# Kernel tuning notes

Hardware: AMD Instinct MI355X
Metric: run time of the kernel (lower is better)

Reference implementation:

```python
import jax, jax.numpy as jnp
import numpy as np

B, C, H, W = 8, 128, 128, 128
WS, NH = 4, 8
HD = C // NH
SCALE = HD ** -0.5
HG, WG = H // WS, W // WS
G, N = HG * WG, WS * WS


def conv2d(x, w, b, padding=0, groups=1):
    out = jax.lax.conv_general_dilated(
        x, w, (1, 1), [(padding, padding)] * 2,
        dimension_numbers=('NCHW', 'OIHW', 'NCHW'),
        feature_group_count=groups)
    return out + b[None, :, None, None]


def dsc(x, dw_w, dw_b, pw_w, pw_b):
    # depthwise 3x3 (groups=C) then pointwise 1x1
    h = conv2d(x, dw_w, dw_b, padding=1, groups=x.shape[1])
    return conv2d(h, pw_w, pw_b)


def _window(t):
    # (B,C,H,W) -> (B,G,NH,N,HD) exactly as torch reshape/permute
    t = t.reshape(B, NH, HD, HG, WS, WG, WS)
    return t.transpose(0, 3, 5, 1, 4, 6, 2).reshape(B, G, NH, N, HD)


def setup_inputs() -> dict:
    key = jax.random.key(0)
    ks = jax.random.split(key, 32)
    s = 0.02
    Cr = max(C // 8, 1)
    d = {
        'x': jax.random.normal(ks[0], (B, C, H, W), jnp.float32),
        'y': jax.random.normal(ks[1], (B, C, H, W), jnp.float32),
        'ca_w1': jax.random.normal(ks[2], (Cr, 2 * C, 1, 1)) * s,
        'ca_b1': jnp.zeros((Cr,)),
        'ca_w2': jax.random.normal(ks[3], (2 * C, Cr, 1, 1)) * s,
        'ca_b2': jnp.zeros((2 * C,)),
        'final_w': jax.random.normal(ks[4], (C, 3 * C, 1, 1)) * s,
        'final_b': jnp.zeros((C,)),
        'bn_g': jnp.ones((C,)),
        'bn_b': jnp.zeros((C,)),
        'bn_m': jnp.zeros((C,)),
        'bn_v': jnp.ones((C,)),
    }
    for i, name in enumerate(['q', 'k', 'v', 'proj']):
        d[name + '_dw_w'] = jax.random.normal(ks[5 + 4 * i], (C, 1, 3, 3)) * s
        d[name + '_dw_b'] = jnp.zeros((C,))
        d[name + '_pw_w'] = jax.random.normal(ks[6 + 4 * i], (C, C, 1, 1)) * s
        d[name + '_pw_b'] = jnp.zeros((C,))
    return d


def reference(x, y, ca_w1, ca_b1, ca_w2, ca_b2,
              q_dw_w, q_dw_b, q_pw_w, q_pw_b,
              k_dw_w, k_dw_b, k_pw_w, k_pw_b,
              v_dw_w, v_dw_b, v_pw_w, v_pw_b,
              proj_dw_w, proj_dw_b, proj_pw_w, proj_pw_b,
              final_w, final_b, bn_g, bn_b, bn_m, bn_v):
    element_wise = x * y
    concat = jnp.concatenate([x, y], axis=1)  # (B,2C,H,W)
    # channel attention (squeeze-excite)
    pooled = concat.mean(axis=(2, 3), keepdims=True)
    h = jax.nn.relu(conv2d(pooled, ca_w1, ca_b1))
    ca = jax.nn.sigmoid(conv2d(h, ca_w2, ca_b2))
    attended = concat * ca
    x_att, y_att = attended[:, :C], attended[:, C:]
    # windowed cross-attention: q from y_att, k/v from x_att
    q = _window(dsc(y_att, q_dw_w, q_dw_b, q_pw_w, q_pw_b))
    k = _window(dsc(x_att, k_dw_w, k_dw_b, k_pw_w, k_pw_b))
    v = _window(dsc(x_att, v_dw_w, v_dw_b, v_pw_w, v_pw_b))
    attn = jnp.einsum('bgnqd,bgnkd->bgnqk', q, k) * SCALE
    attn = jax.nn.softmax(attn, axis=-1)
    out = jnp.einsum('bgnqk,bgnkd->bgnqd', attn, v)  # (B,G,NH,N,HD)
    out = out.transpose(0, 1, 3, 2, 4).reshape(B, HG, WG, WS, WS, C)
    out = out.transpose(0, 1, 3, 2, 4, 5).reshape(B, H, W, C).transpose(0, 3, 1, 2)
    cross = dsc(out, proj_dw_w, proj_dw_b, proj_pw_w, proj_pw_b)
    fused = jnp.concatenate([element_wise, y_att, cross], axis=1)
    z = conv2d(fused, final_w, final_b)
    # BatchNorm in eval mode with running stats
    inv = jax.lax.rsqrt(bn_v + 1e-5)
    z = (z - bn_m[None, :, None, None]) * (inv * bn_g)[None, :, None, None] + bn_b[None, :, None, None]
    return jax.nn.relu(z)
```

## Files before the change

kernel.cpp:

```cpp
#include <hip/hip_runtime.h>

typedef __attribute__((ext_vector_type(8))) short short8;
typedef __attribute__((ext_vector_type(4))) float f32x4;
typedef __attribute__((ext_vector_type(2))) unsigned u32x2;
typedef __attribute__((ext_vector_type(4))) unsigned u32x4;

static constexpr int C_ = 128, H_ = 128, W_ = 128;
static constexpr int HW_ = H_ * W_;
static constexpr int CHW_ = C_ * HW_;

__device__ __forceinline__ unsigned short f2b(float f) {
  union { float f; unsigned u; } cv; cv.f = f;
  unsigned r = cv.u + 0x7FFFu + ((cv.u >> 16) & 1u);
  return (unsigned short)(r >> 16);
}
__device__ __forceinline__ float b2f(unsigned short h) {
  union { unsigned u; float f; } cv; cv.u = ((unsigned)h) << 16;
  return cv.f;
}
__device__ __forceinline__ float uasf(unsigned u) {
  union { unsigned u; float f; } cv; cv.u = u; return cv.f;
}
__device__ __forceinline__ int swzo(int pos, int byteInRow) {
  return pos * 256 + (byteInRow ^ ((pos & 7) << 4));
}

__global__ __launch_bounds__(256) void k_pool(const float* __restrict__ x,
                                              const float* __restrict__ y,
                                              float* __restrict__ sums) {
  int blk = blockIdx.x;
  int b = blk >> 8, c = blk & 255;
  const float* src = (c < C_) ? (x + (size_t)b * CHW_ + (size_t)c * HW_)
                              : (y + (size_t)b * CHW_ + (size_t)(c - C_) * HW_);
  const float4* s4 = (const float4*)src;
  float acc = 0.f;
  for (int i = threadIdx.x; i < HW_ / 4; i += 256) {
    float4 v = s4[i];
    acc += v.x + v.y + v.z + v.w;
  }
  for (int off = 32; off; off >>= 1) acc += __shfl_down(acc, off, 64);
  __shared__ float red[4];
  int lane = threadIdx.x & 63, wv = threadIdx.x >> 6;
  if (lane == 0) red[wv] = acc;
  __syncthreads();
  if (threadIdx.x == 0) sums[blk] = red[0] + red[1] + red[2] + red[3];
}

__global__ __launch_bounds__(256) void k_ca(const float* __restrict__ sums,
                                            const float* __restrict__ w1,
                                            const float* __restrict__ b1,
                                            const float* __restrict__ w2,
                                            const float* __restrict__ b2,
                                            float* __restrict__ ca) {
  int b = blockIdx.x;
  __shared__ float pooled[256];
  __shared__ float hb[16];
  int t = threadIdx.x;
  pooled[t] = sums[b * 256 + t] * (1.f / 16384.f);
  __syncthreads();
  if (t < 16) {
    float s = b1[t];
    for (int j = 0; j < 256; ++j) s += w1[t * 256 + j] * pooled[j];
    hb[t] = fmaxf(s, 0.f);
  }
  __syncthreads();
  float s = b2[t];
  for (int r = 0; r < 16; ++r) s += w2[t * 16 + r] * hb[r];
  ca[b * 256 + t] = 1.f / (1.f + __expf(-s));
}

__global__ __launch_bounds__(128) void k_prep(
    const float* __restrict__ qpw, const float* __restrict__ kpw,
    const float* __restrict__ vpw,
    const float* __restrict__ fw, const float* __restrict__ fb,
    const float* __restrict__ ppw, const float* __restrict__ ppb,
    const float* __restrict__ cab,
    unsigned short* __restrict__ Wb, unsigned short* __restrict__ W2b,
    float* __restrict__ bc) {
  int blk = blockIdx.x, c = threadIdx.x;
  if (blk < 768) {
    int mat = blk >> 7, o = blk & 127;
    float v = 0.f;
    if (mat == 0) v = qpw[o * 128 + c];
    else if (mat == 1) v = kpw[o * 128 + c];
    else if (mat == 2) v = vpw[o * 128 + c];
    else if (mat == 3) {
      float a = 0.f;
      for (int m = 0; m < 128; ++m) a += fw[o * 384 + 256 + m] * ppw[m * 128 + c];
      v = a;
      if (c == 0) {
        float bb = fb[o];
        for (int m = 0; m < 128; ++m) bb += fw[o * 384 + 256 + m] * ppb[m];
        bc[o] = bb;
      }
    } else if (mat == 4) v = fw[o * 384 + c];
    else v = 0.f;
    Wb[((size_t)mat << 14) + o * 128 + c] = f2b(v);
  } else {
    int bb = (blk - 768) >> 7, o = blk & 127;
    W2b[((size_t)bb << 14) + o * 128 + c] =
        f2b(fw[o * 384 + 128 + c] * cab[bb * 256 + 128 + c]);
  }
}

__global__ __launch_bounds__(512, 4) void k_qkv_attn(
    const float* __restrict__ x, const float* __restrict__ y,
    const float* __restrict__ cab,
    const float* __restrict__ qdw, const float* __restrict__ qdb,
    const float* __restrict__ kdw, const float* __restrict__ kdb,
    const float* __restrict__ vdw, const float* __restrict__ vdb,
    const unsigned short* __restrict__ Wqkv,
    const float* __restrict__ qpb, const float* __restrict__ kpb,
    const float* __restrict__ vpb,
    unsigned short* __restrict__ outb) {
  __shared__ __align__(16) char lds[53248];
  constexpr int QS = 0, OS = 0;
  constexpr int AV = 16384, VT = 16384;
  constexpr int AK = 32768, KS = 32768;
  constexpr int HA = 16384;
  constexpr int SCR = 49152;

  const int t = threadIdx.x;
  const int l = t & 63;
  const int w = t >> 6;
  const int lm = l & 15, g = l >> 4;
  const int bs = ((blockIdx.x & 7) << 8) | (blockIdx.x >> 3);
  const int b = bs >> 8, tr = bs & 255;
  const int y0 = (tr >> 3) << 2, x0 = (tr & 7) << 4;
  const int ct = t & 127, rowt = t >> 7;
  const int mtile = w & 3, nbase = (w >> 2) * 64;
  unsigned short* hal = (unsigned short*)(lds + HA);

  auto halo_direct = [&](const float* src) {
    #pragma unroll
    for (int tk = 0; tk < 2; ++tk) {
      int task = t + tk * 512;
      if (task < 768) {
        int c = task & 127, hr = task >> 7;
        int gy = y0 - 1 + hr;
        bool rowok = (unsigned)gy < 128u;
        const float* rsrc = src + (size_t)c * HW_ + (size_t)gy * W_;
        f32x4 v[6];
        #pragma unroll
        for (int ck = 0; ck < 6; ++ck) {
          int gx0 = x0 - 4 + 4 * ck;
          bool ok2 = rowok && ((unsigned)gx0 < 125u);
          v[ck] = ok2 ? *(const f32x4*)(rsrc + gx0) : f32x4{0.f, 0.f, 0.f, 0.f};
        }
        int base = (hr * 128 + c) * 18;
        const float* f = (const float*)v;
        #pragma unroll
        for (int e = 0; e < 9; ++e) {
          unsigned u = (unsigned)f2b(f[2 * e + 3]) |
                       ((unsigned)f2b(f[2 * e + 4]) << 16);
          *(unsigned*)(hal + base + 2 * e) = u;
        }
      }
    }
  };

  auto dw_q = [&](const float* wdw, const float* bdw, const float* cas) {
    const float* wp = wdw + ct * 9;
    float wr[9];
    #pragma unroll
    for (int k2 = 0; k2 < 9; ++k2) wr[k2] = wp[k2];
    float cam = cas[ct], bb = bdw[ct];
    float o[16];
    #pragma unroll
    for (int px = 0; px < 16; ++px) o[px] = 0.f;
    #pragma unroll
    for (int rr = 0; rr < 3; ++rr) {
      int base = ((rowt + rr) * 128 + ct) * 18;
      unsigned rp[9];
      #pragma unroll
      for (int e = 0; e < 9; ++e) rp[e] = *(const unsigned*)(hal + base + 2 * e);
      float rv[18];
      #pragma unroll
      for (int e = 0; e < 9; ++e) {
        rv[2 * e] = uasf(rp[e] << 16);
        rv[2 * e + 1] = uasf(rp[e] & 0xffff0000u);
      }
      #pragma unroll
      for (int px = 0; px < 16; ++px)
        o[px] += rv[px] * wr[3 * rr] + rv[px + 1] * wr[3 * rr + 1] +
                 rv[px + 2] * wr[3 * rr + 2];
    }
    #pragma unroll
    for (int px = 0; px < 16; ++px)
      *(unsigned short*)(lds + QS + swzo(rowt * 16 + px, 2 * ct)) =
          f2b(o[px] * cam + bb);
  };

  auto dw_from_regs = [&](const unsigned* hx, const float* wdw,
                          const float* bdw, float cam, int dstOff) {
    const float* wp = wdw + ct * 9;
    float wr[9];
    #pragma unroll
    for (int k2 = 0; k2 < 9; ++k2) wr[k2] = wp[k2];
    float bb = bdw[ct];
    float o[16];
    #pragma unroll
    for (int px = 0; px < 16; ++px) o[px] = 0.f;
    #pragma unroll
    for (int rr = 0; rr < 3; ++rr) {
      float rv[18];
      #pragma unroll
      for (int e = 0; e < 9; ++e) {
        unsigned pk = hx[rr * 9 + e];
        rv[2 * e] = uasf(pk << 16);
        rv[2 * e + 1] = uasf(pk & 0xffff0000u);
      }
      #pragma unroll
      for (int px = 0; px < 16; ++px)
        o[px] += rv[px] * wr[3 * rr] + rv[px + 1] * wr[3 * rr + 1] +
                 rv[px + 2] * wr[3 * rr + 2];
    }
    #pragma unroll
    for (int px = 0; px < 16; ++px)
      *(unsigned short*)(lds + dstOff + swzo(rowt * 16 + px, 2 * ct)) =
          f2b(o[px] * cam + bb);
  };

  auto afrag_load = [&](int aOff, short8* a) {
    #pragma unroll
    for (int ks = 0; ks < 4; ++ks)
      a[ks] = *(const short8*)(lds + aOff +
                 swzo(mtile * 16 + lm, ks * 64 + g * 16));
  };
  auto gemm_from = [&](const short8* a, const unsigned short* Wm,
                       const float* bias, int dstOff) {
    f32x4 acc[4];
    #pragma unroll
    for (int nt = 0; nt < 4; ++nt) acc[nt] = f32x4{0.f, 0.f, 0.f, 0.f};
    #pragma unroll
    for (int ks = 0; ks < 4; ++ks) {
      short8 wf[4];
      #pragma unroll
      for (int nt = 0; nt < 4; ++nt)
        wf[nt] = *(const short8*)(Wm + (nbase + nt * 16 + lm) * 128 +
                                  ks * 32 + g * 8);
      #pragma unroll
      for (int nt = 0; nt < 4; ++nt)
        acc[nt] = __builtin_amdgcn_mfma_f32_16x16x32_bf16(a[ks], wf[nt], acc[nt], 0, 0, 0);
    }
    #pragma unroll
    for (int nt = 0; nt < 4; ++nt) {
      int ch = nbase + nt * 16 + lm;
      float bv = bias[ch];
      #pragma unroll
      for (int r2 = 0; r2 < 4; ++r2) {
        int pos = mtile * 16 + g * 4 + r2;
        *(unsigned short*)(lds + dstOff + swzo(pos, 2 * ch)) =
            f2b(acc[nt][r2] + bv);
      }
    }
  };
  auto gemm_v_from = [&](const short8* a, const unsigned short* Wm,
                         const float* bias) {
    f32x4 acc[4];
    #pragma unroll
    for (int nt = 0; nt < 4; ++nt) acc[nt] = f32x4{0.f, 0.f, 0.f, 0.f};
    #pragma unroll
    for (int ks = 0; ks < 4; ++ks) {
      short8 wf[4];
      #pragma unroll
      for (int nt = 0; nt < 4; ++nt)
        wf[nt] = *(const short8*)(Wm + (nbase + nt * 16 + lm) * 128 +
                                  ks * 32 + g * 8);
      #pragma unroll
      for (int nt = 0; nt < 4; ++nt)
        acc[nt] = __builtin_amdgcn_mfma_f32_16x16x32_bf16(a[ks], wf[nt], acc[nt], 0, 0, 0);
    }
    #pragma unroll
    for (int nt = 0; nt < 4; ++nt) {
      int ch = nbase + nt * 16 + lm;
      float bv = bias[ch];
      int col = (g * 16 + mtile * 4) ^ ((ch & 7) << 3);
      unsigned lo = (unsigned)f2b(acc[nt][0] + bv) |
                    ((unsigned)f2b(acc[nt][1] + bv) << 16);
      unsigned hi = (unsigned)f2b(acc[nt][2] + bv) |
                    ((unsigned)f2b(acc[nt][3] + bv) << 16);
      *(u32x2*)(lds + VT + ch * 128 + 2 * col) = u32x2{lo, hi};
    }
  };

  const float* cax = cab + b * 256;
  const float* cay = cax + 128;
  const float* xb = x + (size_t)b * CHW_;
  const float* yb = y + (size_t)b * CHW_;

  halo_direct(yb);
  __syncthreads();
  dw_q(qdw, qdb, cay);
  __syncthreads();
  short8 aq[4];
  afrag_load(QS, aq);
  halo_direct(xb);
  __syncthreads();
  gemm_from(aq, Wqkv, qpb, QS);
  __builtin_amdgcn_sched_barrier(0);
  unsigned hx[27];
  #pragma unroll
  for (int rr = 0; rr < 3; ++rr) {
    int base = ((rowt + rr) * 128 + ct) * 18;
    #pragma unroll
    for (int e = 0; e < 9; ++e)
      hx[rr * 9 + e] = *(const unsigned*)(hal + base + 2 * e);
  }
  __syncthreads();
  {
    float cam = cax[ct];
    dw_from_regs(hx, kdw, kdb, cam, AK);
    dw_from_regs(hx, vdw, vdb, cam, AV);
  }
  __syncthreads();
  short8 ak[4], av4[4];
  afrag_load(AK, ak);
  afrag_load(AV, av4);
  __syncthreads();
  gemm_from(ak, Wqkv + 16384, kpb, KS);
  gemm_v_from(av4, Wqkv + 32768, vpb);
  __syncthreads();

  u32x2 oac[4];
  {
    const int h = w;
    const int chb = h * 32;
    char* scr = lds + SCR + w * 512;
    const short8 zz = {};
    #pragma unroll
    for (int wi = 0; wi < 4; ++wi) {
      int rowp = (lm >> 2) * 16 + wi * 4 + (lm & 3);
      short8 avf = zz, bvf = zz;
      if (g < 2) {
        avf = *(const short8*)(lds + KS + swzo(rowp, chb + g * 16));
        bvf = *(const short8*)(lds + QS + swzo(rowp, chb + g * 16));
      }
      f32x4 st = __builtin_amdgcn_mfma_f32_16x16x32_bf16(
          avf, bvf, f32x4{0.f, 0.f, 0.f, 0.f}, 0, 0, 0);
      float s0 = st[0] * 0.25f, s1 = st[1] * 0.25f,
            s2 = st[2] * 0.25f, s3 = st[3] * 0.25f;
      float mx = fmaxf(fmaxf(s0, s1), fmaxf(s2, s3));
      mx = fmaxf(mx, __shfl_xor(mx, 16, 64));
      mx = fmaxf(mx, __shfl_xor(mx, 32, 64));
      float e0 = __expf(s0 - mx), e1 = __expf(s1 - mx),
            e2 = __expf(s2 - mx), e3 = __expf(s3 - mx);
      float sm = e0 + e1 + e2 + e3;
      sm += __shfl_xor(sm, 16, 64);
      sm += __shfl_xor(sm, 32, 64);
      float rl = 1.f / sm;
      unsigned p0 = (unsigned)f2b(e0 * rl) | ((unsigned)f2b(e1 * rl) << 16);
      unsigned p1 = (unsigned)f2b(e2 * rl) | ((unsigned)f2b(e3 * rl) << 16);
      *(u32x2*)(scr + lm * 32 + g * 8) = u32x2{p0, p1};
      short8 pb2 = zz, va = zz;
      if (g < 2) {
        pb2 = *(const short8*)(scr + lm * 32 + g * 16);
        int ch = h * 16 + lm;
        va = *(const short8*)(lds + VT + ch * 128 +
                              2 * ((wi * 16 + g * 8) ^ ((ch & 7) << 3)));
      }
      f32x4 ot = __builtin_amdgcn_mfma_f32_16x16x32_bf16(
          va, pb2, f32x4{0.f, 0.f, 0.f, 0.f}, 0, 0, 0);
      unsigned o0 = (unsigned)f2b(ot[0]) | ((unsigned)f2b(ot[1]) << 16);
      unsigned o1 = (unsigned)f2b(ot[2]) | ((unsigned)f2b(ot[3]) << 16);
      oac[wi] = u32x2{o0, o1};
    }
  }
  __syncthreads();
  {
    const int chb = w * 32;
    #pragma unroll
    for (int wi = 0; wi < 4; ++wi) {
      int rowp = (lm >> 2) * 16 + wi * 4 + (lm & 3);
      *(u32x2*)(lds + OS + swzo(rowp, chb + g * 8)) = oac[wi];
    }
  }
  __syncthreads();
  {
    unsigned short* dst = outb + (size_t)b * CHW_ + (size_t)ct * HW_ +
                          (y0 + rowt) * W_ + x0;
    unsigned v[8];
    #pragma unroll
    for (int j = 0; j < 8; ++j) {
      unsigned lo = *(const unsigned short*)(lds + OS + swzo(rowt * 16 + 2 * j, 2 * ct));
      unsigned hi = *(const unsigned short*)(lds + OS + swzo(rowt * 16 + 2 * j + 1, 2 * ct));
      v[j] = lo | (hi << 16);
    }
    *(u32x4*)(dst) = u32x4{v[0], v[1], v[2], v[3]};
    *(u32x4*)(dst + 8) = u32x4{v[4], v[5], v[6], v[7]};
  }
}

__global__ __launch_bounds__(512, 4) void k_final(
    const float* __restrict__ x, const float* __restrict__ y,
    const unsigned short* __restrict__ outb,
    const float* __restrict__ pdw, const float* __restrict__ pdb,
    const unsigned short* __restrict__ W3,
    const unsigned short* __restrict__ W2b,
    const float* __restrict__ bc,
    const float* __restrict__ bng, const float* __restrict__ bnb,
    const float* __restrict__ bnm, const float* __restrict__ bnv,
    float* __restrict__ outp) {
  __shared__ __align__(16) char lds[50176];
  constexpr int A1 = 0, HA = 16384;

  const int t = threadIdx.x, l = t & 63, w = t >> 6;
  const int lm = l & 15, g = l >> 4;
  const int bs = ((blockIdx.x & 7) << 8) | (blockIdx.x >> 3);
  const int b = bs >> 8, tr = bs & 255;
  const int y0 = (tr >> 3) << 2, x0 = (tr & 7) << 4;
  const int ct = t & 127, rowt = t >> 7;
  unsigned short* hal = (unsigned short*)(lds + HA);
  const int mtile = w & 3, nbase = (w >> 2) * 64;

  f32x4 acc[4];
  #pragma unroll
  for (int nt = 0; nt < 4; ++nt) acc[nt] = f32x4{0.f, 0.f, 0.f, 0.f};

  auto gemm_acc = [&](const unsigned short* Wm) {
    #pragma unroll
    for (int ks = 0; ks < 4; ++ks) {
      short8 wf[4];
      #pragma unroll
      for (int nt = 0; nt < 4; ++nt)
        wf[nt] = *(const short8*)(Wm + (nbase + nt * 16 + lm) * 128 +
                                  ks * 32 + g * 8);
      short8 a = *(const short8*)(lds + A1 +
                   swzo(mtile * 16 + lm, ks * 64 + g * 16));
      #pragma unroll
      for (int nt = 0; nt < 4; ++nt)
        acc[nt] = __builtin_amdgcn_mfma_f32_16x16x32_bf16(a, wf[nt], acc[nt], 0, 0, 0);
    }
  };

  const size_t gbase = (size_t)b * CHW_ + (size_t)ct * HW_ +
                       (size_t)(y0 + rowt) * W_ + x0;

  #pragma unroll
  for (int e = 0; e < 4; ++e) {
    f32x4 xv = *(const f32x4*)(x + gbase + 4 * e);
    f32x4 yv = *(const f32x4*)(y + gbase + 4 * e);
    #pragma unroll
    for (int j = 0; j < 4; ++j)
      *(unsigned short*)(lds + A1 + swzo(rowt * 16 + 4 * e + j, 2 * ct)) =
          f2b(xv[j] * yv[j]);
  }
  #pragma unroll
  for (int tk = 0; tk < 2; ++tk) {
    int task = t + tk * 512;
    if (task < 768) {
      int c = task & 127, hr = task >> 7;
      int gy = y0 - 1 + hr;
      bool rowok = (unsigned)gy < 128u;
      const unsigned short* hsrc =
          outb + (size_t)b * CHW_ + (size_t)c * HW_ + (size_t)gy * W_;
      int base = (hr * 128 + c) * 22;
      #pragma unroll
      for (int e = 0; e < 10; ++e) {
        int gx0 = x0 - 2 + 2 * e;
        bool okp = rowok && ((unsigned)gx0 < 127u);
        unsigned u = okp ? *(const unsigned*)(hsrc + gx0) : 0u;
        *(unsigned*)(hal + base + 2 * e) = u;
      }
    }
  }
  __syncthreads();
  gemm_acc(W3 + 16384);
  __syncthreads();
  #pragma unroll
  for (int e = 0; e < 4; ++e) {
    f32x4 yv = *(const f32x4*)(y + gbase + 4 * e);
    #pragma unroll
    for (int j = 0; j < 4; ++j)
      *(unsigned short*)(lds + A1 + swzo(rowt * 16 + 4 * e + j, 2 * ct)) =
          f2b(yv[j]);
  }
  __syncthreads();
  gemm_acc(W2b + ((size_t)b << 14));
  __syncthreads();
  {
    const float* wp = pdw + ct * 9;
    float wr[9];
    #pragma unroll
    for (int k2 = 0; k2 < 9; ++k2) wr[k2] = wp[k2];
    float bb = pdb[ct];
    #pragma unroll
    for (int hf = 0; hf < 2; ++hf) {
      float o[8];
      #pragma unroll
      for (int px = 0; px < 8; ++px) o[px] = 0.f;
      #pragma unroll
      for (int rr = 0; rr < 3; ++rr) {
        int base = ((rowt + rr) * 128 + ct) * 22 + 8 * hf;
        unsigned rp[6];
        #pragma unroll
        for (int e = 0; e < 6; ++e)
          rp[e] = *(const unsigned*)(hal + base + 2 * e);
        float rv[12];
        #pragma unroll
        for (int e = 0; e < 6; ++e) {
          rv[2 * e] = uasf(rp[e] << 16);
          rv[2 * e + 1] = uasf(rp[e] & 0xffff0000u);
        }
        #pragma unroll
        for (int px = 0; px < 8; ++px)
          o[px] += rv[px + 1] * wr[3 * rr] + rv[px + 2] * wr[3 * rr + 1] +
                   rv[px + 3] * wr[3 * rr + 2];
      }
      #pragma unroll
      for (int px = 0; px < 8; ++px)
        *(unsigned short*)(lds + A1 + swzo(rowt * 16 + hf * 8 + px, 2 * ct)) =
            f2b(o[px] + bb);
    }
  }
  __syncthreads();
  gemm_acc(W3);
  float* fst = (float*)(lds + HA);
  #pragma unroll
  for (int nt = 0; nt < 4; ++nt) {
    int ch = nbase + nt * 16 + lm;
    float zb = bc[ch];
    float inv = rsqrtf(bnv[ch] + 1e-5f);
    float gsc = inv * bng[ch];
    float mm = bnm[ch], ab = bnb[ch];
    #pragma unroll
    for (int r2 = 0; r2 < 4; ++r2) {
      int pos = mtile * 16 + g * 4 + r2;
      float z = acc[nt][r2] + zb;
      z = (z - mm) * gsc + ab;
      fst[pos * 130 + ch] = fmaxf(z, 0.f);
    }
  }
  __syncthreads();
  #pragma unroll
  for (int e4 = 0; e4 < 4; ++e4) {
    f32x4 ov;
    #pragma unroll
    for (int j = 0; j < 4; ++j) ov[j] = fst[(rowt * 16 + e4 * 4 + j) * 130 + ct];
    *(f32x4*)(outp + gbase + 4 * e4) = ov;
  }
}

extern "C" void kernel_launch(void* const* d_in, const int* in_sizes, int n_in,
                              void* d_out, int out_size, void* d_ws, size_t ws_size,
                              hipStream_t stream) {
  const float* x       = (const float*)d_in[0];
  const float* y       = (const float*)d_in[1];
  const float* ca_w1   = (const float*)d_in[2];
  const float* ca_b1   = (const float*)d_in[3];
  const float* ca_w2   = (const float*)d_in[4];
  const float* ca_b2   = (const float*)d_in[5];
  const float* final_w = (const float*)d_in[6];
  const float* final_b = (const float*)d_in[7];
  const float* bn_g    = (const float*)d_in[8];
  const float* bn_b    = (const float*)d_in[9];
  const float* bn_m    = (const float*)d_in[10];
  const float* bn_v    = (const float*)d_in[11];
  const float* q_dw_w  = (const float*)d_in[12];
  const float* q_dw_b  = (const float*)d_in[13];
  const float* q_pw_w  = (const float*)d_in[14];
  const float* q_pw_b  = (const float*)d_in[15];
  const float* k_dw_w  = (const float*)d_in[16];
  const float* k_dw_b  = (const float*)d_in[17];
  const float* k_pw_w  = (const float*)d_in[18];
  const float* k_pw_b  = (const float*)d_in[19];
  const float* v_dw_w  = (const float*)d_in[20];
  const float* v_dw_b  = (const float*)d_in[21];
  const float* v_pw_w  = (const float*)d_in[22];
  const float* v_pw_b  = (const float*)d_in[23];
  const float* p_dw_w  = (const float*)d_in[24];
  const float* p_dw_b  = (const float*)d_in[25];
  const float* p_pw_w  = (const float*)d_in[26];
  const float* p_pw_b  = (const float*)d_in[27];

  char* ws = (char*)d_ws;
  float* sums = (float*)(ws + 0);
  float* cab  = (float*)(ws + 8192);
  unsigned short* Wqkv = (unsigned short*)(ws + 16384);
  unsigned short* W3   = Wqkv + 3 * 16384;
  float* bc   = (float*)(ws + 212992);
  unsigned short* W2b  = (unsigned short*)(ws + 213504);
  unsigned short* outb = (unsigned short*)(ws + (1 << 20));

  k_pool<<<2048, 256, 0, stream>>>(x, y, sums);
  k_ca<<<8, 256, 0, stream>>>(sums, ca_w1, ca_b1, ca_w2, ca_b2, cab);
  k_prep<<<1792, 128, 0, stream>>>(q_pw_w, k_pw_w, v_pw_w, final_w, final_b,
                                   p_pw_w, p_pw_b, cab, Wqkv, W2b, bc);
  k_qkv_attn<<<2048, 512, 0, stream>>>(x, y, cab,
      q_dw_w, q_dw_b, k_dw_w, k_dw_b, v_dw_w, v_dw_b,
      Wqkv, q_pw_b, k_pw_b, v_pw_b, outb);
  k_final<<<2048, 512, 0, stream>>>(x, y, outb,
      p_dw_w, p_dw_b, W3, W2b, bc,
      bn_g, bn_b, bn_m, bn_v, (float*)d_out);
}
```

Before: 376.8 us.

## Halve spatial tiles to 32 pixels with 256-thread blocks in both main kernels

Both fused kernels now process 32-pixel tiles (4x8 for attention, 2x16 for final) with 256 threads and half the LDS, launched as 4096 blocks instead of 2048. The depthwise stage is restructured so each thread computes two output rows from four halo rows, and the V-transpose layout is simplified per window. The block index now puts batch in the low bits. The aim is higher occupancy and better latency hiding. The cost is more halo overhead per pixel (a larger fraction of redundant border loads) and more blocks to schedule.

Result: slower. 427.8 us (+13.5%).

```diff
diff --git a/kernel.cpp b/kernel.cpp
--- a/kernel.cpp
+++ b/kernel.cpp
@@ -13,10 +13,6 @@
   union { float f; unsigned u; } cv; cv.f = f;
   unsigned r = cv.u + 0x7FFFu + ((cv.u >> 16) & 1u);
   return (unsigned short)(r >> 16);
-}
-__device__ __forceinline__ float b2f(unsigned short h) {
-  union { unsigned u; float f; } cv; cv.u = ((unsigned)h) << 16;
-  return cv.f;
 }
 __device__ __forceinline__ float uasf(unsigned u) {
   union { unsigned u; float f; } cv; cv.u = u; return cv.f;
@@ -103,7 +99,7 @@
   }
 }
 
-__global__ __launch_bounds__(512, 4) void k_qkv_attn(
+__global__ __launch_bounds__(256, 6) void k_qkv_attn(
     const float* __restrict__ x, const float* __restrict__ y,
     const float* __restrict__ cab,
     const float* __restrict__ qdw, const float* __restrict__ qdb,
@@ -113,112 +109,133 @@
     const float* __restrict__ qpb, const float* __restrict__ kpb,
     const float* __restrict__ vpb,
     unsigned short* __restrict__ outb) {
-  __shared__ __align__(16) char lds[53248];
+  __shared__ __align__(16) char lds[26624];
   constexpr int QS = 0, OS = 0;
-  constexpr int AV = 16384, VT = 16384;
-  constexpr int AK = 32768, KS = 32768;
-  constexpr int HA = 16384;
-  constexpr int SCR = 49152;
+  constexpr int AV = 8192, VT = 8192;
+  constexpr int AK = 16384, KS = 16384;
+  constexpr int HA = 8192;
+  constexpr int SCR = 24576;
 
   const int t = threadIdx.x;
-  const int l = t & 63;
-  const int w = t >> 6;
+  const int l = t & 63, w = t >> 6;
   const int lm = l & 15, g = l >> 4;
-  const int bs = ((blockIdx.x & 7) << 8) | (blockIdx.x >> 3);
-  const int b = bs >> 8, tr = bs & 255;
-  const int y0 = (tr >> 3) << 2, x0 = (tr & 7) << 4;
-  const int ct = t & 127, rowt = t >> 7;
-  const int mtile = w & 3, nbase = (w >> 2) * 64;
+  const int blk = blockIdx.x;
+  const int b = blk & 7, r = blk >> 3;
+  const int ty = r >> 4, tx = r & 15;
+  const int y0 = ty << 2, x0 = tx << 3;
+  const int ct = t & 127, rt = t >> 7;
+  const int mtile = w & 1, nbase = (w >> 1) * 64;
   unsigned short* hal = (unsigned short*)(lds + HA);
 
   auto halo_direct = [&](const float* src) {
     #pragma unroll
-    for (int tk = 0; tk < 2; ++tk) {
-      int task = t + tk * 512;
-      if (task < 768) {
-        int c = task & 127, hr = task >> 7;
-        int gy = y0 - 1 + hr;
-        bool rowok = (unsigned)gy < 128u;
-        const float* rsrc = src + (size_t)c * HW_ + (size_t)gy * W_;
-        f32x4 v[6];
-        #pragma unroll
-        for (int ck = 0; ck < 6; ++ck) {
-          int gx0 = x0 - 4 + 4 * ck;
-          bool ok2 = rowok && ((unsigned)gx0 < 125u);
-          v[ck] = ok2 ? *(const f32x4*)(rsrc + gx0) : f32x4{0.f, 0.f, 0.f, 0.f};
-        }
-        int base = (hr * 128 + c) * 18;
-        const float* f = (const float*)v;
-        #pragma unroll
-        for (int e = 0; e < 9; ++e) {
-          unsigned u = (unsigned)f2b(f[2 * e + 3]) |
-                       ((unsigned)f2b(f[2 * e + 4]) << 16);
-          *(unsigned*)(hal + base + 2 * e) = u;
-        }
+    for (int tk = 0; tk < 3; ++tk) {
+      int task = t + tk * 256;
+      int c = task & 127, hr = task >> 7;
+      int gy = y0 - 1 + hr;
+      bool rowok = (unsigned)gy < 128u;
+      const float* rsrc = src + (size_t)c * HW_ + (size_t)gy * W_;
+      f32x4 v[4];
+      #pragma unroll
+      for (int ck = 0; ck < 4; ++ck) {
+        int gx0 = x0 - 4 + 4 * ck;
+        bool ok2 = rowok && ((unsigned)gx0 < 125u);
+        v[ck] = ok2 ? *(const f32x4*)(rsrc + gx0) : f32x4{0.f, 0.f, 0.f, 0.f};
+      }
+      int base = task * 10;
+      const float* f = (const float*)v;
+      #pragma unroll
+      for (int e = 0; e < 5; ++e) {
+        unsigned u = (unsigned)f2b(f[2 * e + 3]) |
+                     ((unsigned)f2b(f[2 * e + 4]) << 16);
+        *(unsigned*)(hal + base + 2 * e) = u;
       }
     }
   };
 
-  auto dw_q = [&](const float* wdw, const float* bdw, const float* cas) {
+  auto dw_q2 = [&](const float* wdw, const float* bdw, const float* cas,
+                   int dstOff) {
     const float* wp = wdw + ct * 9;
     float wr[9];
     #pragma unroll
     for (int k2 = 0; k2 < 9; ++k2) wr[k2] = wp[k2];
+    float o0[8], o1[8];
+    #pragma unroll
+    for (int px = 0; px < 8; ++px) { o0[px] = 0.f; o1[px] = 0.f; }
+    #pragma unroll
+    for (int rr = 0; rr < 4; ++rr) {
+      int base = ((2 * rt + rr) * 128 + ct) * 10;
+      float rv[10];
+      #pragma unroll
+      for (int e = 0; e < 5; ++e) {
+        unsigned pk = *(const unsigned*)(hal + base + 2 * e);
+        rv[2 * e] = uasf(pk << 16);
+        rv[2 * e + 1] = uasf(pk & 0xffff0000u);
+      }
+      if (rr < 3) {
+        #pragma unroll
+        for (int px = 0; px < 8; ++px)
+          o0[px] += rv[px] * wr[3 * rr] + rv[px + 1] * wr[3 * rr + 1] +
+                    rv[px + 2] * wr[3 * rr + 2];
+      }
+      if (rr > 0) {
+        int rq = rr - 1;
+        #pragma unroll
+        for (int px = 0; px < 8; ++px)
+          o1[px] += rv[px] * wr[3 * rq] + rv[px + 1] * wr[3 * rq + 1] +
+                    rv[px + 2] * wr[3 * rq + 2];
+      }
+    }
     float cam = cas[ct], bb = bdw[ct];
-    float o[16];
-    #pragma unroll
-    for (int px = 0; px < 16; ++px) o[px] = 0.f;
-    #pragma unroll
-    for (int rr = 0; rr < 3; ++rr) {
-      int base = ((rowt + rr) * 128 + ct) * 18;
-      unsigned rp[9];
-      #pragma unroll
-      for (int e = 0; e < 9; ++e) rp[e] = *(const unsigned*)(hal + base + 2 * e);
-      float rv[18];
-      #pragma unroll
-      for (int e = 0; e < 9; ++e) {
-        rv[2 * e] = uasf(rp[e] << 16);
-        rv[2 * e + 1] = uasf(rp[e] & 0xffff0000u);
-      }
-      #pragma unroll
-      for (int px = 0; px < 16; ++px)
-        o[px] += rv[px] * wr[3 * rr] + rv[px + 1] * wr[3 * rr + 1] +
-                 rv[px + 2] * wr[3 * rr + 2];
-    }
-    #pragma unroll
-    for (int px = 0; px < 16; ++px)
-      *(unsigned short*)(lds + QS + swzo(rowt * 16 + px, 2 * ct)) =
-          f2b(o[px] * cam + bb);
+    #pragma unroll
+    for (int px = 0; px < 8; ++px) {
+      *(unsigned short*)(lds + dstOff + swzo(2 * rt * 8 + px, 2 * ct)) =
+          f2b(o0[px] * cam + bb);
+      *(unsigned short*)(lds + dstOff + swzo((2 * rt + 1) * 8 + px, 2 * ct)) =
+          f2b(o1[px] * cam + bb);
+    }
   };
 
-  auto dw_from_regs = [&](const unsigned* hx, const float* wdw,
-                          const float* bdw, float cam, int dstOff) {
+  auto dw_from_hx = [&](const unsigned* hx, const float* wdw,
+                        const float* bdw, float cam, int dstOff) {
     const float* wp = wdw + ct * 9;
     float wr[9];
     #pragma unroll
     for (int k2 = 0; k2 < 9; ++k2) wr[k2] = wp[k2];
-    float bb = bdw[ct];
-    float o[16];
-    #pragma unroll
-    for (int px = 0; px < 16; ++px) o[px] = 0.f;
-    #pragma unroll
-    for (int rr = 0; rr < 3; ++rr) {
-      float rv[18];
-      #pragma unroll
-      for (int e = 0; e < 9; ++e) {
-        unsigned pk = hx[rr * 9 + e];
+    float o0[8], o1[8];
+    #pragma unroll
+    for (int px = 0; px < 8; ++px) { o0[px] = 0.f; o1[px] = 0.f; }
+    #pragma unroll
+    for (int rr = 0; rr < 4; ++rr) {
+      float rv[10];
+      #pragma unroll
+      for (int e = 0; e < 5; ++e) {
+        unsigned pk = hx[rr * 5 + e];
         rv[2 * e] = uasf(pk << 16);
         rv[2 * e + 1] = uasf(pk & 0xffff0000u);
       }
-      #pragma unroll
-      for (int px = 0; px < 16; ++px)
-        o[px] += rv[px] * wr[3 * rr] + rv[px + 1] * wr[3 * rr + 1] +
-                 rv[px + 2] * wr[3 * rr + 2];
-    }
-    #pragma unroll
-    for (int px = 0; px < 16; ++px)
-      *(unsigned short*)(lds + dstOff + swzo(rowt * 16 + px, 2 * ct)) =
-          f2b(o[px] * cam + bb);
+      if (rr < 3) {
+        #pragma unroll
+        for (int px = 0; px < 8; ++px)
+          o0[px] += rv[px] * wr[3 * rr] + rv[px + 1] * wr[3 * rr + 1] +
+                    rv[px + 2] * wr[3 * rr + 2];
+      }
+      if (rr > 0) {
+        int rq = rr - 1;
+        #pragma unroll
+        for (int px = 0; px < 8; ++px)
+          o1[px] += rv[px] * wr[3 * rq] + rv[px + 1] * wr[3 * rq + 1] +
+                    rv[px + 2] * wr[3 * rq + 2];
+      }
+    }
+    float bb = bdw[ct];
+    #pragma unroll
+    for (int px = 0; px < 8; ++px) {
+      *(unsigned short*)(lds + dstOff + swzo(2 * rt * 8 + px, 2 * ct)) =
+          f2b(o0[px] * cam + bb);
+      *(unsigned short*)(lds + dstOff + swzo((2 * rt + 1) * 8 + px, 2 * ct)) =
+          f2b(o1[px] * cam + bb);
+    }
   };
 
   auto afrag_load = [&](int aOff, short8* a) {
@@ -248,10 +265,10 @@
       int ch = nbase + nt * 16 + lm;
       float bv = bias[ch];
       #pragma unroll
-      for (int r2 = 0; r2 < 4; ++r2) {
-        int pos = mtile * 16 + g * 4 + r2;
+      for (int rr = 0; rr < 4; ++rr) {
+        int pos = mtile * 16 + g * 4 + rr;
         *(unsigned short*)(lds + dstOff + swzo(pos, 2 * ch)) =
-            f2b(acc[nt][r2] + bv);
+            f2b(acc[nt][rr] + bv);
       }
     }
   };
@@ -271,16 +288,17 @@
       for (int nt = 0; nt < 4; ++nt)
         acc[nt] = __builtin_amdgcn_mfma_f32_16x16x32_bf16(a[ks], wf[nt], acc[nt], 0, 0, 0);
     }
+    int win = g & 1;
+    int kpb = mtile * 8 + (g >> 1) * 4;
     #pragma unroll
     for (int nt = 0; nt < 4; ++nt) {
       int ch = nbase + nt * 16 + lm;
       float bv = bias[ch];
-      int col = (g * 16 + mtile * 4) ^ ((ch & 7) << 3);
       unsigned lo = (unsigned)f2b(acc[nt][0] + bv) |
                     ((unsigned)f2b(acc[nt][1] + bv) << 16);
       unsigned hi = (unsigned)f2b(acc[nt][2] + bv) |
                     ((unsigned)f2b(acc[nt][3] + bv) << 16);
-      *(u32x2*)(lds + VT + ch * 128 + 2 * col) = u32x2{lo, hi};
+      *(u32x2*)(lds + VT + win * 4096 + ch * 32 + 2 * kpb) = u32x2{lo, hi};
     }
   };
 
@@ -291,27 +309,26 @@
 
   halo_direct(yb);
   __syncthreads();
-  dw_q(qdw, qdb, cay);
+  dw_q2(qdw, qdb, cay, QS);
   __syncthreads();
   short8 aq[4];
   afrag_load(QS, aq);
   halo_direct(xb);
   __syncthreads();
   gemm_from(aq, Wqkv, qpb, QS);
-  __builtin_amdgcn_sched_barrier(0);
-  unsigned hx[27];
+  unsigned hx[20];
   #pragma unroll
-  for (int rr = 0; rr < 3; ++rr) {
-    int base = ((rowt + rr) * 128 + ct) * 18;
-    #pragma unroll
-    for (int e = 0; e < 9; ++e)
-      hx[rr * 9 + e] = *(const unsigned*)(hal + base + 2 * e);
+  for (int rr = 0; rr < 4; ++rr) {
+    int base = ((2 * rt + rr) * 128 + ct) * 10;
+    #pragma unroll
+    for (int e = 0; e < 5; ++e)
+      hx[rr * 5 + e] = *(const unsigned*)(hal + base + 2 * e);
   }
   __syncthreads();
   {
     float cam = cax[ct];
-    dw_from_regs(hx, kdw, kdb, cam, AK);
-    dw_from_regs(hx, vdw, vdb, cam, AV);
+    dw_from_hx(hx, kdw, kdb, cam, AK);
+    dw_from_hx(hx, vdw, vdb, cam, AV);
   }
   __syncthreads();
   short8 ak[4], av4[4];
@@ -324,13 +341,13 @@
 
   u32x2 oac[4];
   {
-    const int h = w;
-    const int chb = h * 32;
     char* scr = lds + SCR + w * 512;
     const short8 zz = {};
     #pragma unroll
     for (int wi = 0; wi < 4; ++wi) {
-      int rowp = (lm >> 2) * 16 + wi * 4 + (lm & 3);
+      int win = wi & 1, h = w * 2 + (wi >> 1);
+      int chb = h * 32;
+      int rowp = (lm >> 2) * 8 + win * 4 + (lm & 3);
       short8 avf = zz, bvf = zz;
       if (g < 2) {
         avf = *(const short8*)(lds + KS + swzo(rowp, chb + g * 16));
@@ -356,8 +373,7 @@
       if (g < 2) {
         pb2 = *(const short8*)(scr + lm * 32 + g * 16);
         int ch = h * 16 + lm;
-        va = *(const short8*)(lds + VT + ch * 128 +
-                              2 * ((wi * 16 + g * 8) ^ ((ch & 7) << 3)));
+        va = *(const short8*)(lds + VT + win * 4096 + ch * 32 + g * 16);
       }
       f32x4 ot = __builtin_amdgcn_mfma_f32_16x16x32_bf16(
           va, pb2, f32x4{0.f, 0.f, 0.f, 0.f}, 0, 0, 0);
@@ -368,30 +384,32 @@
   }
   __syncthreads();
   {
-    const int chb = w * 32;
     #pragma unroll
     for (int wi = 0; wi < 4; ++wi) {
-      int rowp = (lm >> 2) * 16 + wi * 4 + (lm & 3);
-      *(u32x2*)(lds + OS + swzo(rowp, chb + g * 8)) = oac[wi];
+      int win = wi & 1, h = w * 2 + (wi >> 1);
+      int rowp = (lm >> 2) * 8 + win * 4 + (lm & 3);
+      *(u32x2*)(lds + OS + swzo(rowp, h * 32 + g * 8)) = oac[wi];
     }
   }
   __syncthreads();
   {
-    unsigned short* dst = outb + (size_t)b * CHW_ + (size_t)ct * HW_ +
-                          (y0 + rowt) * W_ + x0;
-    unsigned v[8];
-    #pragma unroll
-    for (int j = 0; j < 8; ++j) {
-      unsigned lo = *(const unsigned short*)(lds + OS + swzo(rowt * 16 + 2 * j, 2 * ct));
-      unsigned hi = *(const unsigned short*)(lds + OS + swzo(rowt * 16 + 2 * j + 1, 2 * ct));
-      v[j] = lo | (hi << 16);
-    }
-    *(u32x4*)(dst) = u32x4{v[0], v[1], v[2], v[3]};
-    *(u32x4*)(dst + 8) = u32x4{v[4], v[5], v[6], v[7]};
-  }
-}
-
-__global__ __launch_bounds__(512, 4) void k_final(
+    unsigned short* dst = outb + (size_t)b * CHW_ + (size_t)ct * HW_;
+    #pragma unroll
+    for (int i = 0; i < 2; ++i) {
+      int py = 2 * rt + i;
+      unsigned v[4];
+      #pragma unroll
+      for (int j = 0; j < 4; ++j) {
+        unsigned lo = *(const unsigned short*)(lds + OS + swzo(py * 8 + 2 * j, 2 * ct));
+        unsigned hi = *(const unsigned short*)(lds + OS + swzo(py * 8 + 2 * j + 1, 2 * ct));
+        v[j] = lo | (hi << 16);
+      }
+      *(u32x4*)(dst + (size_t)(y0 + py) * W_ + x0) = u32x4{v[0], v[1], v[2], v[3]};
+    }
+  }
+}
+
+__global__ __launch_bounds__(256, 5) void k_final(
     const float* __restrict__ x, const float* __restrict__ y,
     const unsigned short* __restrict__ outb,
     const float* __restrict__ pdw, const float* __restrict__ pdb,
@@ -401,17 +419,19 @@
     const float* __restrict__ bng, const float* __restrict__ bnb,
     const float* __restrict__ bnm, const float* __restrict__ bnv,
     float* __restrict__ outp) {
-  __shared__ __align__(16) char lds[50176];
-  constexpr int A1 = 0, HA = 16384;
-
-  const int t = threadIdx.x, l = t & 63, w = t >> 6;
+  __shared__ __align__(16) char lds[28672];
+  constexpr int A1 = 0, HA = 8192;
+
+  const int t = threadIdx.x;
+  const int l = t & 63, w = t >> 6;
   const int lm = l & 15, g = l >> 4;
-  const int bs = ((blockIdx.x & 7) << 8) | (blockIdx.x >> 3);
-  const int b = bs >> 8, tr = bs & 255;
-  const int y0 = (tr >> 3) << 2, x0 = (tr & 7) << 4;
-  const int ct = t & 127, rowt = t >> 7;
+  const int blk = blockIdx.x;
+  const int b = blk & 7, r = blk >> 3;
+  const int ty = r >> 3, tx = r & 7;
+  const int y0 = ty << 1, x0 = tx << 4;
+  const int ct = t & 127, rt = t >> 7;
   unsigned short* hal = (unsigned short*)(lds + HA);
-  const int mtile = w & 3, nbase = (w >> 2) * 64;
+  const int mtile = w & 1, nbase = (w >> 1) * 64;
 
   f32x4 acc[4];
   #pragma unroll
@@ -434,7 +454,7 @@
   };
 
   const size_t gbase = (size_t)b * CHW_ + (size_t)ct * HW_ +
-                       (size_t)(y0 + rowt) * W_ + x0;
+                       (size_t)(y0 + rt) * W_ + x0;
 
   #pragma unroll
   for (int e = 0; e < 4; ++e) {
@@ -442,26 +462,24 @@
     f32x4 yv = *(const f32x4*)(y + gbase + 4 * e);
     #pragma unroll
     for (int j = 0; j < 4; ++j)
-      *(unsigned short*)(lds + A1 + swzo(rowt * 16 + 4 * e + j, 2 * ct)) =
+      *(unsigned short*)(lds + A1 + swzo(rt * 16 + 4 * e + j, 2 * ct)) =
           f2b(xv[j] * yv[j]);
   }
   #pragma unroll
   for (int tk = 0; tk < 2; ++tk) {
-    int task = t + tk * 512;
-    if (task < 768) {
-      int c = task & 127, hr = task >> 7;
-      int gy = y0 - 1 + hr;
-      bool rowok = (unsigned)gy < 128u;
-      const unsigned short* hsrc =
-          outb + (size_t)b * CHW_ + (size_t)c * HW_ + (size_t)gy * W_;
-      int base = (hr * 128 + c) * 22;
-      #pragma unroll
-      for (int e = 0; e < 10; ++e) {
-        int gx0 = x0 - 2 + 2 * e;
-        bool okp = rowok && ((unsigned)gx0 < 127u);
-        unsigned u = okp ? *(const unsigned*)(hsrc + gx0) : 0u;
-        *(unsigned*)(hal + base + 2 * e) = u;
-      }
+    int task = t + tk * 256;
+    int c = task & 127, hr = task >> 7;
+    int gy = y0 - 1 + hr;
+    bool rowok = (unsigned)gy < 128u;
+    const unsigned short* hsrc =
+        outb + (size_t)b * CHW_ + (size_t)c * HW_ + (size_t)gy * W_;
+    int base = task * 20;
+    #pragma unroll
+    for (int e = 0; e < 10; ++e) {
+      int gx0 = x0 - 2 + 2 * e;
+      bool okp = rowok && ((unsigned)gx0 < 127u);
+      unsigned u = okp ? *(const unsigned*)(hsrc + gx0) : 0u;
+      *(unsigned*)(hal + base + 2 * e) = u;
     }
   }
   __syncthreads();
@@ -472,7 +490,7 @@
     f32x4 yv = *(const f32x4*)(y + gbase + 4 * e);
     #pragma unroll
     for (int j = 0; j < 4; ++j)
-      *(unsigned short*)(lds + A1 + swzo(rowt * 16 + 4 * e + j, 2 * ct)) =
+      *(unsigned short*)(lds + A1 + swzo(rt * 16 + 4 * e + j, 2 * ct)) =
           f2b(yv[j]);
   }
   __syncthreads();
@@ -484,34 +502,28 @@
     #pragma unroll
     for (int k2 = 0; k2 < 9; ++k2) wr[k2] = wp[k2];
     float bb = pdb[ct];
-    #pragma unroll
-    for (int hf = 0; hf < 2; ++hf) {
-      float o[8];
-      #pragma unroll
-      for (int px = 0; px < 8; ++px) o[px] = 0.f;
-      #pragma unroll
-      for (int rr = 0; rr < 3; ++rr) {
-        int base = ((rowt + rr) * 128 + ct) * 22 + 8 * hf;
-        unsigned rp[6];
-        #pragma unroll
-        for (int e = 0; e < 6; ++e)
-          rp[e] = *(const unsigned*)(hal + base + 2 * e);
-        float rv[12];
-        #pragma unroll
-        for (int e = 0; e < 6; ++e) {
-          rv[2 * e] = uasf(rp[e] << 16);
-          rv[2 * e + 1] = uasf(rp[e] & 0xffff0000u);
-        }
-        #pragma unroll
-        for (int px = 0; px < 8; ++px)
-          o[px] += rv[px + 1] * wr[3 * rr] + rv[px + 2] * wr[3 * rr + 1] +
-                   rv[px + 3] * wr[3 * rr + 2];
-      }
-      #pragma unroll
-      for (int px = 0; px < 8; ++px)
-        *(unsigned short*)(lds + A1 + swzo(rowt * 16 + hf * 8 + px, 2 * ct)) =
-            f2b(o[px] + bb);
-    }
+    float o[16];
+    #pragma unroll
+    for (int px = 0; px < 16; ++px) o[px] = 0.f;
+    #pragma unroll
+    for (int rr = 0; rr < 3; ++rr) {
+      int base = ((rt + rr) * 128 + ct) * 20;
+      float rv[20];
+      #pragma unroll
+      for (int e = 0; e < 10; ++e) {
+        unsigned pk = *(const unsigned*)(hal + base + 2 * e);
+        rv[2 * e] = uasf(pk << 16);
+        rv[2 * e + 1] = uasf(pk & 0xffff0000u);
+      }
+      #pragma unroll
+      for (int px = 0; px < 16; ++px)
+        o[px] += rv[px + 1] * wr[3 * rr] + rv[px + 2] * wr[3 * rr + 1] +
+                 rv[px + 3] * wr[3 * rr + 2];
+    }
+    #pragma unroll
+    for (int px = 0; px < 16; ++px)
+      *(unsigned short*)(lds + A1 + swzo(rt * 16 + px, 2 * ct)) =
+          f2b(o[px] + bb);
   }
   __syncthreads();
   gemm_acc(W3);
@@ -524,9 +536,9 @@
     float gsc = inv * bng[ch];
     float mm = bnm[ch], ab = bnb[ch];
     #pragma unroll
-    for (int r2 = 0; r2 < 4; ++r2) {
-      int pos = mtile * 16 + g * 4 + r2;
-      float z = acc[nt][r2] + zb;
+    for (int rr = 0; rr < 4; ++rr) {
+      int pos = mtile * 16 + g * 4 + rr;
+      float z = acc[nt][rr] + zb;
       z = (z - mm) * gsc + ab;
       fst[pos * 130 + ch] = fmaxf(z, 0.f);
     }
@@ -536,7 +548,7 @@
   for (int e4 = 0; e4 < 4; ++e4) {
     f32x4 ov;
     #pragma unroll
-    for (int j = 0; j < 4; ++j) ov[j] = fst[(rowt * 16 + e4 * 4 + j) * 130 + ct];
+    for (int j = 0; j < 4; ++j) ov[j] = fst[(rt * 16 + e4 * 4 + j) * 130 + ct];
     *(f32x4*)(outp + gbase + 4 * e4) = ov;
   }
 }
@@ -586,10 +598,10 @@
   k_ca<<<8, 256, 0, stream>>>(sums, ca_w1, ca_b1, ca_w2, ca_b2, cab);
   k_prep<<<1792, 128, 0, stream>>>(q_pw_w, k_pw_w, v_pw_w, final_w, final_b,
                                    p_pw_w, p_pw_b, cab, Wqkv, W2b, bc);
-  k_qkv_attn<<<2048, 512, 0, stream>>>(x, y, cab,
+  k_qkv_attn<<<4096, 256, 0, stream>>>(x, y, cab,
       q_dw_w, q_dw_b, k_dw_w, k_dw_b, v_dw_w, v_dw_b,
       Wqkv, q_pw_b, k_pw_b, v_pw_b, outb);
-  k_final<<<2048, 512, 0, stream>>>(x, y, outb,
+  k_final<<<4096, 256, 0, stream>>>(x, y, outb,
       p_dw_w, p_dw_b, W3, W2b, bc,
       bn_g, bn_b, bn_m, bn_v, (float*)d_out);
 }
```
